# Performance work log

Hardware: AMD Instinct MI355X
Metric: run time of the kernel (lower is better)

The kernel has to match this reference:

```python
import jax, jax.numpy as jnp
import numpy as np
import math

B, H, S, D = 2, 16, 2048, 128

def setup_inputs() -> dict:
    key = jax.random.key(0)
    k1, k2, k3, k4 = jax.random.split(key, 4)
    x1 = jax.random.normal(k1, (B, H, S, D), dtype=jnp.float32)
    x2 = jax.random.normal(k2, (B, H, S, D), dtype=jnp.float32)
    x3 = jax.random.normal(k3, (B, H, D, S), dtype=jnp.float32)
    attn_mask = jax.random.normal(k4, (S, S), dtype=jnp.float32)
    return {"x1": x1, "x2": x2, "x3": x3, "attn_mask": attn_mask}

def reference(x1, x2, x3, attn_mask):
    scale = 1.0 / math.sqrt(x1.shape[-1])
    # [B,H,S,S] scores
    qk = jnp.einsum('bhqd,bhkd->bhqk', x1, x2) * scale + attn_mask
    attn_weight = jax.nn.softmax(qk, axis=-1)
    # x3 @ attn_weight : [B,H,D,S] @ [B,H,S,S] -> [B,H,D,S]
    output = jnp.einsum('bhds,bhsk->bhdk', x3, attn_weight)
    return output
```

## Files before the change

kernel.cpp:

```cpp
#include <hip/hip_runtime.h>


typedef __attribute__((ext_vector_type(8))) short short8;
typedef __attribute__((ext_vector_type(4))) float f32x4;

#define S_LEN 2048
#define D_LEN 128
#define BH_N 32
#define SCALE_QK 0.08838834764831845f
#define LOG2E 1.4426950408889634f

__device__ __forceinline__ unsigned short f2bf(float f) {
    union { float f; unsigned int i; } v; v.f = f;
    unsigned int r = v.i + 0x7FFFu + ((v.i >> 16) & 1u);
    return (unsigned short)(r >> 16);
}
__device__ __forceinline__ float bf2f(unsigned short u) {
    union { unsigned int i; float f; } v; v.i = ((unsigned int)u) << 16; return v.f;
}
__device__ __forceinline__ uint2 pack4bf(float4 v) {
    uint2 p;
    p.x = (unsigned)f2bf(v.x) | ((unsigned)f2bf(v.y) << 16);
    p.y = (unsigned)f2bf(v.z) | ((unsigned)f2bf(v.w) << 16);
    return p;
}
__device__ __forceinline__ unsigned cvt_pk_bf16(float lo, float hi) {
    unsigned r;
    asm("v_cvt_pk_bf16_f32 %0, %1, %2" : "=v"(r) : "v"(lo), "v"(hi));
    return r;
}

__global__ void k_cvt(const float* __restrict__ x1,
                      const float* __restrict__ x2,
                      const float* __restrict__ mask,
                      unsigned short* __restrict__ x1s,
                      unsigned short* __restrict__ x2b,
                      unsigned short* __restrict__ mbf) {
    const size_t N1 = (size_t)BH_N * S_LEN * D_LEN;
    const size_t NM = (size_t)S_LEN * S_LEN;
    size_t i = ((size_t)blockIdx.x * 256 + threadIdx.x) * 4;
    const float s1 = SCALE_QK * LOG2E;
    if (i < N1) {
        float4 v = *(const float4*)&x1[i];
        v.x *= s1; v.y *= s1; v.z *= s1; v.w *= s1;
        *(uint2*)&x1s[i] = pack4bf(v);
    } else if (i < 2 * N1) {
        size_t j = i - N1;
        float4 v = *(const float4*)&x2[j];
        *(uint2*)&x2b[j] = pack4bf(v);
    } else if (i < 2 * N1 + NM) {
        size_t j = i - 2 * N1;
        float4 v = *(const float4*)&mask[j];
        v.x *= LOG2E; v.y *= LOG2E; v.z *= LOG2E; v.w *= LOG2E;
        *(uint2*)&mbf[j] = pack4bf(v);
    }
}

__global__ __launch_bounds__(256, 2) void k_qk(
    const unsigned short* __restrict__ x1s,
    const unsigned short* __restrict__ x2b,
    const unsigned short* __restrict__ mbf,
    const float* __restrict__ x3,
    unsigned short* __restrict__ x3s)
{
    __shared__ unsigned short sQ[128 * 128];
    __shared__ unsigned short sK[128 * 128];
    __shared__ float sRL[128];
    const int q0 = blockIdx.x * 128;
    const int bh = blockIdx.y;
    const unsigned short* x1p = x1s + (size_t)bh * S_LEN * D_LEN;
    const unsigned short* x2p = x2b + (size_t)bh * S_LEN * D_LEN;
    const int t = threadIdx.x;
    const int w = t >> 6, lane = t & 63, quad = lane >> 4, l16 = lane & 15;

#pragma unroll
    for (int i = 0; i < 8; ++i) {
        int idx = i * 256 + t;
        int r = idx >> 4, c = idx & 15;
        *(uint4*)&sQ[r * 128 + ((c ^ (r & 7)) * 8)] =
            *(const uint4*)&x1p[(size_t)(q0 + r) * D_LEN + c * 8];
    }

    float rs[8] = {0.f, 0.f, 0.f, 0.f, 0.f, 0.f, 0.f, 0.f};

    for (int k0 = 0; k0 < S_LEN; k0 += 128) {
        __syncthreads();
#pragma unroll
        for (int i = 0; i < 8; ++i) {
            int idx = i * 256 + t;
            int r = idx >> 4, c = idx & 15;
            *(uint4*)&sK[r * 128 + ((c ^ (r & 7)) * 8)] =
                *(const uint4*)&x2p[(size_t)(k0 + r) * D_LEN + c * 8];
        }
        __syncthreads();

        unsigned short mpf[2][8][4];
#pragma unroll
        for (int qb = 0; qb < 2; ++qb)
#pragma unroll
            for (int kb = 0; kb < 8; ++kb)
#pragma unroll
                for (int rr = 0; rr < 4; ++rr)
                    mpf[qb][kb][rr] =
                        mbf[(size_t)(q0 + 32 * w + 16 * qb + 4 * quad + rr) * S_LEN
                            + k0 + kb * 16 + l16];

        f32x4 acc[2][8];
#pragma unroll
        for (int qb = 0; qb < 2; ++qb)
#pragma unroll
            for (int kb = 0; kb < 8; ++kb) acc[qb][kb] = (f32x4){0.f, 0.f, 0.f, 0.f};

        __builtin_amdgcn_s_setprio(1);
#pragma unroll
        for (int kk = 0; kk < 4; ++kk) {
            const int sc = ((kk * 4 + quad) ^ (l16 & 7)) * 8;
            short8 a[2];
#pragma unroll
            for (int qb = 0; qb < 2; ++qb)
                a[qb] = *(const short8*)&sQ[(32 * w + 16 * qb + l16) * 128 + sc];
            short8 b[8];
#pragma unroll
            for (int kb = 0; kb < 8; ++kb)
                b[kb] = *(const short8*)&sK[(kb * 16 + l16) * 128 + sc];
#pragma unroll
            for (int qb = 0; qb < 2; ++qb)
#pragma unroll
                for (int kb = 0; kb < 8; ++kb)
                    acc[qb][kb] = __builtin_amdgcn_mfma_f32_16x16x32_bf16(a[qb], b[kb], acc[qb][kb], 0, 0, 0);
        }
        __builtin_amdgcn_s_setprio(0);

#pragma unroll
        for (int qb = 0; qb < 2; ++qb)
#pragma unroll
            for (int kb = 0; kb < 8; ++kb)
#pragma unroll
                for (int rr = 0; rr < 4; ++rr)
                    rs[qb * 4 + rr] += exp2f(acc[qb][kb][rr] + bf2f(mpf[qb][kb][rr]));
    }

#pragma unroll
    for (int i = 0; i < 8; ++i) {
        float v = rs[i];
        v += __shfl_xor(v, 1); v += __shfl_xor(v, 2);
        v += __shfl_xor(v, 4); v += __shfl_xor(v, 8);
        if (l16 == 0) sRL[32 * w + 16 * (i >> 2) + 4 * quad + (i & 3)] = 1.0f / v;
    }
    __syncthreads();

    const float* x3b = x3 + (size_t)bh * (size_t)D_LEN * S_LEN;
    unsigned short* x3sp = x3s + (size_t)bh * (size_t)D_LEN * S_LEN;
#pragma unroll
    for (int i = 0; i < 16; ++i) {
        int e = (i * 256 + t) * 4;
        int r = e >> 7, c = e & 127;
        float4 v = *(const float4*)&x3b[(size_t)r * S_LEN + q0 + c];
        v.x *= sRL[c]; v.y *= sRL[c + 1]; v.z *= sRL[c + 2]; v.w *= sRL[c + 3];
        *(uint2*)&x3sp[(size_t)r * S_LEN + q0 + c] = pack4bf(v);
    }
}

__global__ __launch_bounds__(256, 2) void k_out(
    const unsigned short* __restrict__ x1s,
    const unsigned short* __restrict__ x2b,
    const unsigned short* __restrict__ x3s,
    const unsigned short* __restrict__ mbf,
    float* __restrict__ out)
{
    __shared__ unsigned short sK[128 * 128];
    __shared__ unsigned short sQ[64 * 128];
    __shared__ unsigned short sX[128 * 64];
    __shared__ unsigned short sE[128 * 64];
    const int kb0 = blockIdx.x * 128;
    const int bh = blockIdx.y;
    const unsigned short* x1p = x1s + (size_t)bh * S_LEN * D_LEN;
    const unsigned short* x2p = x2b + (size_t)bh * S_LEN * D_LEN;
    const unsigned short* x3p = x3s + (size_t)bh * (size_t)D_LEN * S_LEN;
    const int t = threadIdx.x;
    const int w = t >> 6, lane = t & 63, quad = lane >> 4, l16 = lane & 15;
    const int qrow = 16 * w + 4 * quad;
    const int cE = qrow >> 3;
    const int qoff7 = qrow & 7;

#pragma unroll
    for (int i = 0; i < 8; ++i) {
        int idx = i * 256 + t;
        int r = idx >> 4, c = idx & 15;
        *(uint4*)&sK[r * 128 + ((c ^ (r & 7)) * 8)] =
            *(const uint4*)&x2p[(size_t)(kb0 + r) * D_LEN + c * 8];
    }

    f32x4 oa[16];
#pragma unroll
    for (int i = 0; i < 16; ++i) oa[i] = (f32x4){0.f, 0.f, 0.f, 0.f};

    for (int q0 = 0; q0 < S_LEN; q0 += 64) {
        __syncthreads();
#pragma unroll
        for (int i = 0; i < 4; ++i) {
            int idx = i * 256 + t;
            int r = idx >> 4, c = idx & 15;
            *(uint4*)&sQ[r * 128 + ((c ^ (r & 7)) * 8)] =
                *(const uint4*)&x1p[(size_t)(q0 + r) * D_LEN + c * 8];
        }
#pragma unroll
        for (int i = 0; i < 4; ++i) {
            int idx = i * 256 + t;
            int r = idx >> 3, c = idx & 7;
            *(uint4*)&sX[r * 64 + ((c ^ (r & 7)) * 8)] =
                *(const uint4*)&x3p[(size_t)r * S_LEN + q0 + c * 8];
        }
        __syncthreads();

        unsigned short mpf[8][4];
#pragma unroll
        for (int kb = 0; kb < 8; ++kb)
#pragma unroll
            for (int rr = 0; rr < 4; ++rr)
                mpf[kb][rr] = mbf[(size_t)(q0 + qrow + rr) * S_LEN + kb0 + kb * 16 + l16];

        f32x4 acc[8];
#pragma unroll
        for (int kb = 0; kb < 8; ++kb) acc[kb] = (f32x4){0.f, 0.f, 0.f, 0.f};
        __builtin_amdgcn_s_setprio(1);
#pragma unroll
        for (int kk = 0; kk < 4; ++kk) {
            const int sc = ((kk * 4 + quad) ^ (l16 & 7)) * 8;
            short8 a = *(const short8*)&sQ[(16 * w + l16) * 128 + sc];
            short8 b[8];
#pragma unroll
            for (int kb = 0; kb < 8; ++kb)
                b[kb] = *(const short8*)&sK[(kb * 16 + l16) * 128 + sc];
#pragma unroll
            for (int kb = 0; kb < 8; ++kb)
                acc[kb] = __builtin_amdgcn_mfma_f32_16x16x32_bf16(a, b[kb], acc[kb], 0, 0, 0);
        }
        __builtin_amdgcn_s_setprio(0);

#pragma unroll
        for (int kb = 0; kb < 8; ++kb) {
            float e0 = exp2f(acc[kb][0] + bf2f(mpf[kb][0]));
            float e1 = exp2f(acc[kb][1] + bf2f(mpf[kb][1]));
            float e2 = exp2f(acc[kb][2] + bf2f(mpf[kb][2]));
            float e3 = exp2f(acc[kb][3] + bf2f(mpf[kb][3]));
            uint2 pk;
            pk.x = cvt_pk_bf16(e0, e1);
            pk.y = cvt_pk_bf16(e2, e3);
            const int krow = kb * 16 + l16;
            *(uint2*)&sE[krow * 64 + ((cE ^ (krow & 7)) * 8) + qoff7] = pk;
        }
        __syncthreads();

        __builtin_amdgcn_s_setprio(1);
#pragma unroll
        for (int kk = 0; kk < 2; ++kk) {
            const int sc = ((kk * 4 + quad) ^ (l16 & 7)) * 8;
            short8 a[2];
#pragma unroll
            for (int db = 0; db < 2; ++db)
                a[db] = *(const short8*)&sX[(32 * w + 16 * db + l16) * 64 + sc];
            short8 b[8];
#pragma unroll
            for (int kb = 0; kb < 8; ++kb)
                b[kb] = *(const short8*)&sE[(kb * 16 + l16) * 64 + sc];
#pragma unroll
            for (int db = 0; db < 2; ++db)
#pragma unroll
                for (int kb = 0; kb < 8; ++kb)
                    oa[db * 8 + kb] = __builtin_amdgcn_mfma_f32_16x16x32_bf16(a[db], b[kb], oa[db * 8 + kb], 0, 0, 0);
        }
        __builtin_amdgcn_s_setprio(0);
    }

#pragma unroll
    for (int db = 0; db < 2; ++db)
#pragma unroll
        for (int kb = 0; kb < 8; ++kb)
#pragma unroll
            for (int rr = 0; rr < 4; ++rr) {
                int d = 32 * w + 16 * db + 4 * quad + rr;
                out[((size_t)bh * D_LEN + d) * S_LEN + kb0 + kb * 16 + l16] =
                    oa[db * 8 + kb][rr];
            }
}

__global__ __launch_bounds__(256, 3) void k_rowsum_fb(
    const float* __restrict__ x1, const float* __restrict__ x2,
    const float* __restrict__ mask, float* __restrict__ rl)
{
    __shared__ unsigned short sQ[128 * 136];
    __shared__ unsigned short sK[64 * 136];
    const int q0 = blockIdx.x * 128;
    const int bh = blockIdx.y;
    const float* x1b = x1 + (size_t)bh * S_LEN * D_LEN;
    const float* x2b = x2 + (size_t)bh * S_LEN * D_LEN;
    const int t = threadIdx.x;
    const int w = t >> 6, lane = t & 63, quad = lane >> 4, l16 = lane & 15;
#pragma unroll
    for (int i = 0; i < 16; ++i) {
        int e = (i * 256 + t) * 4;
        int r = e >> 7, c = e & 127;
        float4 v = *(const float4*)&x1b[(size_t)(q0 + r) * D_LEN + c];
        *(uint2*)&sQ[r * 136 + c] = pack4bf(v);
    }
    float rs[8] = {0.f, 0.f, 0.f, 0.f, 0.f, 0.f, 0.f, 0.f};
    for (int k0 = 0; k0 < S_LEN; k0 += 64) {
        __syncthreads();
#pragma unroll
        for (int i = 0; i < 8; ++i) {
            int e = (i * 256 + t) * 4;
            int r = e >> 7, c = e & 127;
            float4 v = *(const float4*)&x2b[(size_t)(k0 + r) * D_LEN + c];
            *(uint2*)&sK[r * 136 + c] = pack4bf(v);
        }
        __syncthreads();
#pragma unroll
        for (int qb = 0; qb < 2; ++qb) {
            const int qrow = 32 * w + 16 * qb;
#pragma unroll
            for (int kb = 0; kb < 4; ++kb) {
                f32x4 acc = {0.f, 0.f, 0.f, 0.f};
#pragma unroll
                for (int kk = 0; kk < 4; ++kk) {
                    short8 a = *(const short8*)&sQ[(qrow + l16) * 136 + kk * 32 + quad * 8];
                    short8 b = *(const short8*)&sK[(kb * 16 + l16) * 136 + kk * 32 + quad * 8];
                    acc = __builtin_amdgcn_mfma_f32_16x16x32_bf16(a, b, acc, 0, 0, 0);
                }
                const int kg = k0 + kb * 16 + l16;
                const int qg = q0 + qrow + 4 * quad;
#pragma unroll
                for (int r = 0; r < 4; ++r) {
                    float m = mask[(size_t)(qg + r) * S_LEN + kg];
                    rs[qb * 4 + r] += __expf(acc[r] * SCALE_QK + m);
                }
            }
        }
    }
#pragma unroll
    for (int i = 0; i < 8; ++i) {
        float v = rs[i];
        v += __shfl_xor(v, 1); v += __shfl_xor(v, 2);
        v += __shfl_xor(v, 4); v += __shfl_xor(v, 8);
        if (l16 == 0) {
            int qg = q0 + 32 * w + 16 * (i >> 2) + 4 * quad + (i & 3);
            rl[(size_t)bh * S_LEN + qg] = 1.0f / v;
        }
    }
}

__global__ __launch_bounds__(256, 2) void k_out_fb(
    const float* __restrict__ x1, const float* __restrict__ x2,
    const float* __restrict__ x3, const float* __restrict__ mask,
    const float* __restrict__ rl, float* __restrict__ out)
{
    __shared__ unsigned short sK[64 * 136];
    __shared__ unsigned short sQ[64 * 136];
    __shared__ unsigned short sX[128 * 72];
    __shared__ unsigned short sE[64 * 72];
    const int kb0 = blockIdx.x * 64;
    const int bh = blockIdx.y;
    const float* x1b = x1 + (size_t)bh * S_LEN * D_LEN;
    const float* x2b = x2 + (size_t)bh * S_LEN * D_LEN;
    const float* x3b = x3 + (size_t)bh * (size_t)D_LEN * S_LEN;
    const float* rlb = rl + (size_t)bh * S_LEN;
    const int t = threadIdx.x;
    const int w = t >> 6, lane = t & 63, quad = lane >> 4, l16 = lane & 15;
#pragma unroll
    for (int i = 0; i < 8; ++i) {
        int e = (i * 256 + t) * 4;
        int r = e >> 7, c = e & 127;
        float4 v = *(const float4*)&x2b[(size_t)(kb0 + r) * D_LEN + c];
        *(uint2*)&sK[r * 136 + c] = pack4bf(v);
    }
    f32x4 oa[8];
#pragma unroll
    for (int i = 0; i < 8; ++i) oa[i] = (f32x4){0.f, 0.f, 0.f, 0.f};
    for (int q0 = 0; q0 < S_LEN; q0 += 64) {
        __syncthreads();
#pragma unroll
        for (int i = 0; i < 8; ++i) {
            int e = (i * 256 + t) * 4;
            int r = e >> 7, c = e & 127;
            float4 v = *(const float4*)&x1b[(size_t)(q0 + r) * D_LEN + c];
            *(uint2*)&sQ[r * 136 + c] = pack4bf(v);
        }
#pragma unroll
        for (int i = 0; i < 8; ++i) {
            int e = (i * 256 + t) * 4;
            int r = e >> 6, c = e & 63;
            float4 v = *(const float4*)&x3b[(size_t)r * S_LEN + q0 + c];
            *(uint2*)&sX[r * 72 + c] = pack4bf(v);
        }
        __syncthreads();
        const int qrow = 16 * w + 4 * quad;
        float rl4[4];
#pragma unroll
        for (int r = 0; r < 4; ++r) rl4[r] = rlb[q0 + qrow + r];
#pragma unroll
        for (int kb = 0; kb < 4; ++kb) {
            f32x4 acc = {0.f, 0.f, 0.f, 0.f};
#pragma unroll
            for (int kk = 0; kk < 4; ++kk) {
                short8 a = *(const short8*)&sQ[(16 * w + l16) * 136 + kk * 32 + quad * 8];
                short8 b = *(const short8*)&sK[(kb * 16 + l16) * 136 + kk * 32 + quad * 8];
                acc = __builtin_amdgcn_mfma_f32_16x16x32_bf16(a, b, acc, 0, 0, 0);
            }
            const int kg = kb0 + kb * 16 + l16;
            unsigned short e4[4];
#pragma unroll
            for (int r = 0; r < 4; ++r) {
                float m = mask[(size_t)(q0 + qrow + r) * S_LEN + kg];
                e4[r] = f2bf(__expf(acc[r] * SCALE_QK + m) * rl4[r]);
            }
            uint2 pk;
            pk.x = (unsigned)e4[0] | ((unsigned)e4[1] << 16);
            pk.y = (unsigned)e4[2] | ((unsigned)e4[3] << 16);
            *(uint2*)&sE[(kb * 16 + l16) * 72 + qrow] = pk;
        }
        __syncthreads();
#pragma unroll
        for (int db = 0; db < 2; ++db)
#pragma unroll
            for (int kb = 0; kb < 4; ++kb) {
                f32x4 a0 = oa[db * 4 + kb];
#pragma unroll
                for (int kk = 0; kk < 2; ++kk) {
                    short8 a = *(const short8*)&sX[(32 * w + 16 * db + l16) * 72 + kk * 32 + quad * 8];
                    short8 b = *(const short8*)&sE[(kb * 16 + l16) * 72 + kk * 32 + quad * 8];
                    a0 = __builtin_amdgcn_mfma_f32_16x16x32_bf16(a, b, a0, 0, 0, 0);
                }
                oa[db * 4 + kb] = a0;
            }
    }
#pragma unroll
    for (int db = 0; db < 2; ++db)
#pragma unroll
        for (int kb = 0; kb < 4; ++kb)
#pragma unroll
            for (int r = 0; r < 4; ++r) {
                int d = 32 * w + 16 * db + 4 * quad + r;
                out[((size_t)bh * D_LEN + d) * S_LEN + kb0 + kb * 16 + l16] =
                    oa[db * 4 + kb][r];
            }
}

extern "C" void kernel_launch(void* const* d_in, const int* in_sizes, int n_in,
                              void* d_out, int out_size, void* d_ws, size_t ws_size,
                              hipStream_t stream) {
    const float* x1 = (const float*)d_in[0];
    const float* x2 = (const float*)d_in[1];
    const float* x3 = (const float*)d_in[2];
    const float* mask = (const float*)d_in[3];
    float* out = (float*)d_out;

    const size_t N1 = (size_t)BH_N * S_LEN * D_LEN;
    const size_t NM = (size_t)S_LEN * S_LEN;
    const size_t need = (3 * N1 + NM) * sizeof(unsigned short);

    if (ws_size >= need) {
        unsigned short* x1s = (unsigned short*)d_ws;
        unsigned short* x2b = x1s + N1;
        unsigned short* x3s = x2b + N1;
        unsigned short* mbf = x3s + N1;
        const size_t tot4 = (2 * N1 + NM) / 4;
        k_cvt<<<dim3((unsigned)(tot4 / 256)), dim3(256), 0, stream>>>(x1, x2, mask, x1s, x2b, mbf);
        k_qk<<<dim3(S_LEN / 128, BH_N), dim3(256), 0, stream>>>(x1s, x2b, mbf, x3, x3s);
        k_out<<<dim3(S_LEN / 128, BH_N), dim3(256), 0, stream>>>(x1s, x2b, x3s, mbf, out);
    } else {
        float* rl = (float*)d_ws;
        k_rowsum_fb<<<dim3(S_LEN / 128, BH_N), dim3(256), 0, stream>>>(x1, x2, mask, rl);
        k_out_fb<<<dim3(S_LEN / 64, BH_N), dim3(256), 0, stream>>>(x1, x2, x3, mask, rl, out);
    }
}
```

Measured before the change: 310.6 us.

## Load Q and X3 MFMA operands directly from global into registers, reorder grid

Measured after the change: 462.7 us. +49.0%, slower.

```diff
diff --git a/kernel.cpp b/kernel.cpp
--- a/kernel.cpp
+++ b/kernel.cpp
@@ -23,11 +23,6 @@
     p.x = (unsigned)f2bf(v.x) | ((unsigned)f2bf(v.y) << 16);
     p.y = (unsigned)f2bf(v.z) | ((unsigned)f2bf(v.w) << 16);
     return p;
-}
-__device__ __forceinline__ unsigned cvt_pk_bf16(float lo, float hi) {
-    unsigned r;
-    asm("v_cvt_pk_bf16_f32 %0, %1, %2" : "=v"(r) : "v"(lo), "v"(hi));
-    return r;
 }
 
 __global__ void k_cvt(const float* __restrict__ x1,
@@ -56,30 +51,29 @@
     }
 }
 
-__global__ __launch_bounds__(256, 2) void k_qk(
+__global__ __launch_bounds__(256, 3) void k_qk(
     const unsigned short* __restrict__ x1s,
     const unsigned short* __restrict__ x2b,
     const unsigned short* __restrict__ mbf,
     const float* __restrict__ x3,
     unsigned short* __restrict__ x3s)
 {
-    __shared__ unsigned short sQ[128 * 128];
     __shared__ unsigned short sK[128 * 128];
     __shared__ float sRL[128];
-    const int q0 = blockIdx.x * 128;
-    const int bh = blockIdx.y;
+    const int bh = blockIdx.x;
+    const int q0 = blockIdx.y * 128;
     const unsigned short* x1p = x1s + (size_t)bh * S_LEN * D_LEN;
     const unsigned short* x2p = x2b + (size_t)bh * S_LEN * D_LEN;
     const int t = threadIdx.x;
     const int w = t >> 6, lane = t & 63, quad = lane >> 4, l16 = lane & 15;
 
-#pragma unroll
-    for (int i = 0; i < 8; ++i) {
-        int idx = i * 256 + t;
-        int r = idx >> 4, c = idx & 15;
-        *(uint4*)&sQ[r * 128 + ((c ^ (r & 7)) * 8)] =
-            *(const uint4*)&x1p[(size_t)(q0 + r) * D_LEN + c * 8];
-    }
+    short8 aq[2][4];
+#pragma unroll
+    for (int qb = 0; qb < 2; ++qb)
+#pragma unroll
+        for (int kk = 0; kk < 4; ++kk)
+            aq[qb][kk] = *(const short8*)&x1p[(size_t)(q0 + 32 * w + 16 * qb + l16) * D_LEN
+                                              + (kk * 4 + quad) * 8];
 
     float rs[8] = {0.f, 0.f, 0.f, 0.f, 0.f, 0.f, 0.f, 0.f};
 
@@ -94,31 +88,15 @@
         }
         __syncthreads();
 
-        unsigned short mpf[2][8][4];
+        f32x4 acc[2][8];
 #pragma unroll
         for (int qb = 0; qb < 2; ++qb)
 #pragma unroll
-            for (int kb = 0; kb < 8; ++kb)
-#pragma unroll
-                for (int rr = 0; rr < 4; ++rr)
-                    mpf[qb][kb][rr] =
-                        mbf[(size_t)(q0 + 32 * w + 16 * qb + 4 * quad + rr) * S_LEN
-                            + k0 + kb * 16 + l16];
-
-        f32x4 acc[2][8];
-#pragma unroll
-        for (int qb = 0; qb < 2; ++qb)
-#pragma unroll
             for (int kb = 0; kb < 8; ++kb) acc[qb][kb] = (f32x4){0.f, 0.f, 0.f, 0.f};
 
-        __builtin_amdgcn_s_setprio(1);
 #pragma unroll
         for (int kk = 0; kk < 4; ++kk) {
             const int sc = ((kk * 4 + quad) ^ (l16 & 7)) * 8;
-            short8 a[2];
-#pragma unroll
-            for (int qb = 0; qb < 2; ++qb)
-                a[qb] = *(const short8*)&sQ[(32 * w + 16 * qb + l16) * 128 + sc];
             short8 b[8];
 #pragma unroll
             for (int kb = 0; kb < 8; ++kb)
@@ -127,17 +105,19 @@
             for (int qb = 0; qb < 2; ++qb)
 #pragma unroll
                 for (int kb = 0; kb < 8; ++kb)
-                    acc[qb][kb] = __builtin_amdgcn_mfma_f32_16x16x32_bf16(a[qb], b[kb], acc[qb][kb], 0, 0, 0);
-        }
-        __builtin_amdgcn_s_setprio(0);
+                    acc[qb][kb] = __builtin_amdgcn_mfma_f32_16x16x32_bf16(aq[qb][kk], b[kb], acc[qb][kb], 0, 0, 0);
+        }
 
 #pragma unroll
         for (int qb = 0; qb < 2; ++qb)
 #pragma unroll
-            for (int kb = 0; kb < 8; ++kb)
+            for (int kb = 0; kb < 8; ++kb) {
+                const size_t mrow = (size_t)(q0 + 32 * w + 16 * qb + 4 * quad) * S_LEN
+                                    + k0 + kb * 16 + l16;
 #pragma unroll
                 for (int rr = 0; rr < 4; ++rr)
-                    rs[qb * 4 + rr] += exp2f(acc[qb][kb][rr] + bf2f(mpf[qb][kb][rr]));
+                    rs[qb * 4 + rr] += exp2f(acc[qb][kb][rr] + bf2f(mbf[mrow + (size_t)rr * S_LEN]));
+            }
     }
 
 #pragma unroll
@@ -161,7 +141,7 @@
     }
 }
 
-__global__ __launch_bounds__(256, 2) void k_out(
+__global__ __launch_bounds__(256, 3) void k_out(
     const unsigned short* __restrict__ x1s,
     const unsigned short* __restrict__ x2b,
     const unsigned short* __restrict__ x3s,
@@ -169,11 +149,9 @@
     float* __restrict__ out)
 {
     __shared__ unsigned short sK[128 * 128];
-    __shared__ unsigned short sQ[64 * 128];
-    __shared__ unsigned short sX[128 * 64];
     __shared__ unsigned short sE[128 * 64];
-    const int kb0 = blockIdx.x * 128;
-    const int bh = blockIdx.y;
+    const int bh = blockIdx.x;
+    const int kb0 = blockIdx.y * 128;
     const unsigned short* x1p = x1s + (size_t)bh * S_LEN * D_LEN;
     const unsigned short* x2p = x2b + (size_t)bh * S_LEN * D_LEN;
     const unsigned short* x3p = x3s + (size_t)bh * (size_t)D_LEN * S_LEN;
@@ -195,71 +173,62 @@
 #pragma unroll
     for (int i = 0; i < 16; ++i) oa[i] = (f32x4){0.f, 0.f, 0.f, 0.f};
 
+    __syncthreads();
+
     for (int q0 = 0; q0 < S_LEN; q0 += 64) {
-        __syncthreads();
-#pragma unroll
-        for (int i = 0; i < 4; ++i) {
-            int idx = i * 256 + t;
-            int r = idx >> 4, c = idx & 15;
-            *(uint4*)&sQ[r * 128 + ((c ^ (r & 7)) * 8)] =
-                *(const uint4*)&x1p[(size_t)(q0 + r) * D_LEN + c * 8];
-        }
-#pragma unroll
-        for (int i = 0; i < 4; ++i) {
-            int idx = i * 256 + t;
-            int r = idx >> 3, c = idx & 7;
-            *(uint4*)&sX[r * 64 + ((c ^ (r & 7)) * 8)] =
-                *(const uint4*)&x3p[(size_t)r * S_LEN + q0 + c * 8];
-        }
-        __syncthreads();
-
-        unsigned short mpf[8][4];
-#pragma unroll
-        for (int kb = 0; kb < 8; ++kb)
-#pragma unroll
-            for (int rr = 0; rr < 4; ++rr)
-                mpf[kb][rr] = mbf[(size_t)(q0 + qrow + rr) * S_LEN + kb0 + kb * 16 + l16];
+        short8 aq[4];
+#pragma unroll
+        for (int kk = 0; kk < 4; ++kk)
+            aq[kk] = *(const short8*)&x1p[(size_t)(q0 + 16 * w + l16) * D_LEN
+                                           + (kk * 4 + quad) * 8];
 
         f32x4 acc[8];
 #pragma unroll
         for (int kb = 0; kb < 8; ++kb) acc[kb] = (f32x4){0.f, 0.f, 0.f, 0.f};
-        __builtin_amdgcn_s_setprio(1);
 #pragma unroll
         for (int kk = 0; kk < 4; ++kk) {
             const int sc = ((kk * 4 + quad) ^ (l16 & 7)) * 8;
-            short8 a = *(const short8*)&sQ[(16 * w + l16) * 128 + sc];
             short8 b[8];
 #pragma unroll
             for (int kb = 0; kb < 8; ++kb)
                 b[kb] = *(const short8*)&sK[(kb * 16 + l16) * 128 + sc];
 #pragma unroll
             for (int kb = 0; kb < 8; ++kb)
-                acc[kb] = __builtin_amdgcn_mfma_f32_16x16x32_bf16(a, b[kb], acc[kb], 0, 0, 0);
-        }
-        __builtin_amdgcn_s_setprio(0);
-
+                acc[kb] = __builtin_amdgcn_mfma_f32_16x16x32_bf16(aq[kk], b[kb], acc[kb], 0, 0, 0);
+        }
+
+        uint2 pk[8];
 #pragma unroll
         for (int kb = 0; kb < 8; ++kb) {
-            float e0 = exp2f(acc[kb][0] + bf2f(mpf[kb][0]));
-            float e1 = exp2f(acc[kb][1] + bf2f(mpf[kb][1]));
-            float e2 = exp2f(acc[kb][2] + bf2f(mpf[kb][2]));
-            float e3 = exp2f(acc[kb][3] + bf2f(mpf[kb][3]));
-            uint2 pk;
-            pk.x = cvt_pk_bf16(e0, e1);
-            pk.y = cvt_pk_bf16(e2, e3);
+            const size_t mrow = (size_t)(q0 + qrow) * S_LEN + kb0 + kb * 16 + l16;
+            float e0 = exp2f(acc[kb][0] + bf2f(mbf[mrow]));
+            float e1 = exp2f(acc[kb][1] + bf2f(mbf[mrow + S_LEN]));
+            float e2 = exp2f(acc[kb][2] + bf2f(mbf[mrow + 2 * S_LEN]));
+            float e3 = exp2f(acc[kb][3] + bf2f(mbf[mrow + 3 * S_LEN]));
+            pk[kb].x = (unsigned)f2bf(e0) | ((unsigned)f2bf(e1) << 16);
+            pk[kb].y = (unsigned)f2bf(e2) | ((unsigned)f2bf(e3) << 16);
+        }
+
+        __syncthreads();
+#pragma unroll
+        for (int kb = 0; kb < 8; ++kb) {
             const int krow = kb * 16 + l16;
-            *(uint2*)&sE[krow * 64 + ((cE ^ (krow & 7)) * 8) + qoff7] = pk;
-        }
-        __syncthreads();
-
-        __builtin_amdgcn_s_setprio(1);
+            *(uint2*)&sE[krow * 64 + ((cE ^ (krow & 7)) * 8) + qoff7] = pk[kb];
+        }
+
+        short8 ax[2][2];
+#pragma unroll
+        for (int db = 0; db < 2; ++db)
+#pragma unroll
+            for (int kk = 0; kk < 2; ++kk)
+                ax[db][kk] = *(const short8*)&x3p[(size_t)(32 * w + 16 * db + l16) * S_LEN
+                                                  + q0 + (kk * 4 + quad) * 8];
+
+        __syncthreads();
+
 #pragma unroll
         for (int kk = 0; kk < 2; ++kk) {
             const int sc = ((kk * 4 + quad) ^ (l16 & 7)) * 8;
-            short8 a[2];
-#pragma unroll
-            for (int db = 0; db < 2; ++db)
-                a[db] = *(const short8*)&sX[(32 * w + 16 * db + l16) * 64 + sc];
             short8 b[8];
 #pragma unroll
             for (int kb = 0; kb < 8; ++kb)
@@ -268,9 +237,8 @@
             for (int db = 0; db < 2; ++db)
 #pragma unroll
                 for (int kb = 0; kb < 8; ++kb)
-                    oa[db * 8 + kb] = __builtin_amdgcn_mfma_f32_16x16x32_bf16(a[db], b[kb], oa[db * 8 + kb], 0, 0, 0);
-        }
-        __builtin_amdgcn_s_setprio(0);
+                    oa[db * 8 + kb] = __builtin_amdgcn_mfma_f32_16x16x32_bf16(ax[db][kk], b[kb], oa[db * 8 + kb], 0, 0, 0);
+        }
     }
 
 #pragma unroll
@@ -465,8 +433,8 @@
         unsigned short* mbf = x3s + N1;
         const size_t tot4 = (2 * N1 + NM) / 4;
         k_cvt<<<dim3((unsigned)(tot4 / 256)), dim3(256), 0, stream>>>(x1, x2, mask, x1s, x2b, mbf);
-        k_qk<<<dim3(S_LEN / 128, BH_N), dim3(256), 0, stream>>>(x1s, x2b, mbf, x3, x3s);
-        k_out<<<dim3(S_LEN / 128, BH_N), dim3(256), 0, stream>>>(x1s, x2b, x3s, mbf, out);
+        k_qk<<<dim3(BH_N, S_LEN / 128), dim3(256), 0, stream>>>(x1s, x2b, mbf, x3, x3s);
+        k_out<<<dim3(BH_N, S_LEN / 128), dim3(256), 0, stream>>>(x1s, x2b, x3s, mbf, out);
     } else {
         float* rl = (float*)d_ws;
         k_rowsum_fb<<<dim3(S_LEN / 128, BH_N), dim3(256), 0, stream>>>(x1, x2, mask, rl);
```
